# Performance work log

Measured on AMD Instinct MI355X. Metric: run time of the kernel, lower is better.

The kernel has to match this reference:

```python
import jax, jax.numpy as jnp
import numpy as np

N, IN_DIM, HID, HEADS = 4096, 256, 64, 8


def setup_inputs() -> dict:
    key = jax.random.key(0)
    ks = jax.random.split(key, 9)
    feats = jax.random.normal(ks[0], (N, IN_DIM), dtype=jnp.float32)
    adj = jax.random.bernoulli(ks[1], 0.01, (N, N)) | jnp.eye(N, dtype=bool)
    def lin(k, fin, fout):
        return jax.random.normal(k, (fin, fout), dtype=jnp.float32) / np.float32(np.sqrt(fin))
    return {
        "features": feats,
        "adjacency": adj,
        "W_in": lin(ks[2], IN_DIM, HID * HEADS),            # linear (no bias)
        "W_out": lin(ks[3], HID * HEADS, HID),              # out_proj
        "b_out": jnp.zeros((HID,), jnp.float32),
        "W_c1": lin(ks[4], HID * 2, HID),                   # classifier[1]
        "b_c1": jnp.zeros((HID,), jnp.float32),
        "W_c2": lin(ks[5], HID, 1),                         # classifier[3]
        "b_c2": jnp.zeros((1,), jnp.float32),
    }


def reference(features, adjacency, W_in, W_out, b_out, W_c1, b_c1, W_c2, b_c2):
    n = features.shape[0]
    # multi-head GAT: [H, N, D]
    proj = (features @ W_in).reshape(n, HEADS, HID).transpose(1, 0, 2)
    logits = jnp.einsum('hnd,hmd->hnm', proj, proj) / np.float32(np.sqrt(HID))
    logits = jnp.where(adjacency[None, :, :], logits, -jnp.inf)
    attn = jax.nn.softmax(logits, axis=-1)
    attended = jnp.einsum('hnm,hmd->hnd', attn, proj)
    attended = attended.transpose(1, 0, 2).reshape(n, HEADS * HID)
    node_states = attended @ W_out + b_out
    # memory_bank is None -> concat with zeros
    fused = jnp.concatenate([node_states, jnp.zeros_like(node_states)], axis=-1)
    h = jax.nn.gelu(fused, approximate=False) @ W_c1 + b_c1
    scores = (jax.nn.gelu(h, approximate=False) @ W_c2 + b_c2).squeeze(-1)
    # attention heatmap: masked row-normalized cosine similarity
    eps = np.float32(1e-8)
    norm = jnp.maximum(jnp.linalg.norm(node_states, axis=-1, keepdims=True), eps)
    xn = node_states / norm
    sim = jnp.where(adjacency, xn @ xn.T, 0.0)
    heatmap = sim / (sim.sum(axis=-1, keepdims=True) + eps)
    return scores, heatmap
```

## Files before the change

kernel.cpp:

```cpp
#include <hip/hip_runtime.h>
#include <math.h>

constexpr int NN    = 4096;
constexpr int INDIM = 256;
constexpr int HID   = 64;
constexpr int HEADS = 8;
constexpr int HH    = HID * HEADS;
constexpr int DMAX  = 256;
constexpr int PROJ_BLOCKS = 512;

typedef float        vfloat4 __attribute__((ext_vector_type(4)));
typedef unsigned int vuint4  __attribute__((ext_vector_type(4)));

__device__ __forceinline__ float gelu_exact(float x) {
    return 0.5f * x * (1.0f + erff(x * 0.70710678118654752f));
}

__device__ __forceinline__ float wave_reduce64(float v) {
    v += __shfl_xor(v, 32); v += __shfl_xor(v, 16); v += __shfl_xor(v, 8);
    v += __shfl_xor(v, 4);  v += __shfl_xor(v, 2);  v += __shfl_xor(v, 1);
    return v;
}

__global__ __launch_bounds__(256) void prep_kernel(
    const void* __restrict__ adjv,
    const float* __restrict__ A, const float* __restrict__ B,
    float* __restrict__ projT,
    unsigned short* __restrict__ nbr_g, int* __restrict__ deg_g) {
    __shared__ float Bs[128][64];
    __shared__ int wsum[4], u8w[4];
    const int pb = blockIdx.x, t = threadIdx.x;
    const int wv = t >> 6, lane = t & 63;

    if (pb < PROJ_BLOCKS) {
        const int bx = pb & 7, by = pb >> 3;
        const int tx = t & 15, ty = t >> 4;
        const float* ap0 = A + (size_t)(by * 64 + ty * 4 + 0) * INDIM;
        const float* ap1 = A + (size_t)(by * 64 + ty * 4 + 1) * INDIM;
        const float* ap2 = A + (size_t)(by * 64 + ty * 4 + 2) * INDIM;
        const float* ap3 = A + (size_t)(by * 64 + ty * 4 + 3) * INDIM;
        float acc[4][4] = {{0.0f}};

        for (int kh = 0; kh < 2; ++kh) {
            #pragma unroll
            for (int i = t; i < 128 * 16; i += 256) {
                const int k = i >> 4, c4 = (i & 15) * 4;
                *reinterpret_cast<float4*>(&Bs[k][c4]) =
                    *reinterpret_cast<const float4*>(
                        B + (size_t)(kh * 128 + k) * HH + bx * 64 + c4);
            }
            __syncthreads();
            #pragma unroll 2
            for (int k = 0; k < 128; k += 4) {
                const int ka = kh * 128 + k;
                float4 av[4];
                av[0] = *reinterpret_cast<const float4*>(ap0 + ka);
                av[1] = *reinterpret_cast<const float4*>(ap1 + ka);
                av[2] = *reinterpret_cast<const float4*>(ap2 + ka);
                av[3] = *reinterpret_cast<const float4*>(ap3 + ka);
                float4 bv[4];
                #pragma unroll
                for (int kk = 0; kk < 4; ++kk)
                    bv[kk] = *reinterpret_cast<const float4*>(&Bs[k + kk][tx * 4]);
                #pragma unroll
                for (int i = 0; i < 4; ++i) {
                    const float a0 = av[i].x, a1 = av[i].y, a2 = av[i].z, a3 = av[i].w;
                    acc[i][0] += a0 * bv[0].x + a1 * bv[1].x + a2 * bv[2].x + a3 * bv[3].x;
                    acc[i][1] += a0 * bv[0].y + a1 * bv[1].y + a2 * bv[2].y + a3 * bv[3].y;
                    acc[i][2] += a0 * bv[0].z + a1 * bv[1].z + a2 * bv[2].z + a3 * bv[3].z;
                    acc[i][3] += a0 * bv[0].w + a1 * bv[1].w + a2 * bv[2].w + a3 * bv[3].w;
                }
            }
            __syncthreads();
        }
        #pragma unroll
        for (int i = 0; i < 4; ++i) {
            float4 o = {acc[i][0], acc[i][1], acc[i][2], acc[i][3]};
            *reinterpret_cast<float4*>(
                projT + ((size_t)bx * NN + by * 64 + ty * 4 + i) * HID + tx * 4) = o;
        }
    } else {
        const int n = pb - PROJ_BLOCKS;
        const vuint4 pw = __builtin_nontemporal_load(
            reinterpret_cast<const vuint4*>(adjv) + t);
        int u8loc = 0;
        #pragma unroll
        for (int a = 0; a < 4; ++a) {
            const unsigned w = pw[a];
            if (((w & ~0x01010101u) == 0u) && ((w & 0xFFFFFF00u) != 0u)) u8loc = 1;
        }
        const unsigned long long wb = __ballot(u8loc);
        if (lane == 0) u8w[wv] = (wb != 0ull);
        __syncthreads();
        const bool isU8 = (u8w[0] | u8w[1] | u8w[2] | u8w[3]) != 0;

        unsigned int nzmask = 0;
        if (isU8) {
            const vuint4 r = __builtin_nontemporal_load(
                reinterpret_cast<const vuint4*>(
                    (const unsigned char*)adjv + (size_t)n * NN + 16 * t));
            #pragma unroll
            for (int a = 0; a < 4; ++a)
                #pragma unroll
                for (int j = 0; j < 4; ++j)
                    if ((r[a] >> (8 * j)) & 0xFFu) nzmask |= 1u << (a * 4 + j);
        } else {
            const vuint4* p = reinterpret_cast<const vuint4*>(
                (const unsigned int*)adjv + (size_t)n * NN + 16 * t);
            #pragma unroll
            for (int a = 0; a < 4; ++a) {
                const vuint4 r = __builtin_nontemporal_load(p + a);
                if (r[0]) nzmask |= 1u << (a * 4 + 0);
                if (r[1]) nzmask |= 1u << (a * 4 + 1);
                if (r[2]) nzmask |= 1u << (a * 4 + 2);
                if (r[3]) nzmask |= 1u << (a * 4 + 3);
            }
        }
        const int c = __popc(nzmask);
        int x = c;
        #pragma unroll
        for (int d = 1; d < 64; d <<= 1) {
            int y = __shfl_up(x, d);
            if (lane >= d) x += y;
        }
        if (lane == 63) wsum[wv] = x;
        __syncthreads();
        int base = 0;
        #pragma unroll
        for (int i = 0; i < 4; ++i)
            if (i < wv) base += wsum[i];
        const int deg = min(wsum[0] + wsum[1] + wsum[2] + wsum[3], DMAX);
        if (t == 0) deg_g[n] = deg;
        int o = base + x - c;
        unsigned int mm = nzmask;
        while (mm) {
            const int j = __ffs(mm) - 1;
            mm &= mm - 1;
            if (o < DMAX) nbr_g[(size_t)n * DMAX + o] = (unsigned short)(16 * t + j);
            ++o;
        }
    }
}

__global__ __launch_bounds__(256) void attn_kernel(
    const float* __restrict__ projT,
    const unsigned short* __restrict__ nbr_g, const int* __restrict__ deg_g,
    float* __restrict__ attended) {
    __shared__ unsigned short nl[4][DMAX];
    const int b = blockIdx.x, t = threadIdx.x;
    const int wv = t >> 6, lane = t & 63;
    const int h = b & 7;
    const int n = (b >> 3) * 4 + wv;
    const int deg = deg_g[n];

    *reinterpret_cast<ushort4*>(&nl[wv][lane * 4]) =
        *reinterpret_cast<const ushort4*>(nbr_g + (size_t)n * DMAX + lane * 4);

    const float* tab = projT + (size_t)h * NN * HID;
    const int g = lane >> 3, dl = (lane & 7) * 8;

    float q[8];
    {
        const float4 a = *reinterpret_cast<const float4*>(tab + (size_t)n * HID + dl);
        const float4 bq = *reinterpret_cast<const float4*>(tab + (size_t)n * HID + dl + 4);
        q[0] = a.x;  q[1] = a.y;  q[2] = a.z;  q[3] = a.w;
        q[4] = bq.x; q[5] = bq.y; q[6] = bq.z; q[7] = bq.w;
    }

    float l = 0.0f;
    float acc[8] = {0.f, 0.f, 0.f, 0.f, 0.f, 0.f, 0.f, 0.f};
    #pragma unroll 2
    for (int c0 = 0; c0 < deg; c0 += 8) {
        const int c = c0 + g;
        const int idx = nl[wv][min(c, deg - 1)];
        const float* kp = tab + (size_t)idx * HID + dl;
        const float4 ka = *reinterpret_cast<const float4*>(kp);
        const float4 kb = *reinterpret_cast<const float4*>(kp + 4);
        float kf[8] = {ka.x, ka.y, ka.z, ka.w, kb.x, kb.y, kb.z, kb.w};
        float s = q[0]*kf[0] + q[1]*kf[1] + q[2]*kf[2] + q[3]*kf[3] +
                  q[4]*kf[4] + q[5]*kf[5] + q[6]*kf[6] + q[7]*kf[7];
        s += __shfl_xor(s, 1); s += __shfl_xor(s, 2); s += __shfl_xor(s, 4);
        const float w = (c < deg) ? expf(s * 0.125f) : 0.0f;
        l += w;
        #pragma unroll
        for (int i = 0; i < 8; ++i) acc[i] += w * kf[i];
    }
    l += __shfl_xor(l, 8); l += __shfl_xor(l, 16); l += __shfl_xor(l, 32);
    #pragma unroll
    for (int i = 0; i < 8; ++i) {
        acc[i] += __shfl_xor(acc[i], 8);
        acc[i] += __shfl_xor(acc[i], 16);
        acc[i] += __shfl_xor(acc[i], 32);
    }
    const float invL = 1.0f / l;
    if (g == 0) {
        float4 o1 = {acc[0] * invL, acc[1] * invL, acc[2] * invL, acc[3] * invL};
        float4 o2 = {acc[4] * invL, acc[5] * invL, acc[6] * invL, acc[7] * invL};
        float* dst = attended + (size_t)n * HH + h * HID + dl;
        *reinterpret_cast<float4*>(dst)     = o1;
        *reinterpret_cast<float4*>(dst + 4) = o2;
    }
}

__global__ __launch_bounds__(256) void post_kernel(
    const float* __restrict__ attended,
    const float* __restrict__ W_out, const float* __restrict__ b_out,
    const float* __restrict__ W_c1, const float* __restrict__ b_c1,
    const float* __restrict__ W_c2, const float* __restrict__ b_c2,
    float* __restrict__ scores, float* __restrict__ xn) {
    __shared__ float qv2[4][HH];
    __shared__ float red[4][16][HID];
    __shared__ float nsbuf[4][HID];
    const int n0 = blockIdx.x * 4, t = threadIdx.x;
    const int wv = t >> 6, lane = t & 63;

    #pragma unroll
    for (int nd = 0; nd < 4; ++nd) {
        qv2[nd][t]       = attended[(size_t)(n0 + nd) * HH + t];
        qv2[nd][t + 256] = attended[(size_t)(n0 + nd) * HH + t + 256];
    }
    __syncthreads();

    {
        const int part = t >> 4, jq = (t & 15) * 4;
        float4 p0 = {0,0,0,0}, p1 = {0,0,0,0}, p2 = {0,0,0,0}, p3 = {0,0,0,0};
        const int d0 = part * 32;
        #pragma unroll 4
        for (int d = d0; d < d0 + 32; ++d) {
            const float4 w4 = *reinterpret_cast<const float4*>(&W_out[d * HID + jq]);
            const float q0 = qv2[0][d], q1 = qv2[1][d];
            const float q2 = qv2[2][d], q3 = qv2[3][d];
            p0.x += q0 * w4.x; p0.y += q0 * w4.y; p0.z += q0 * w4.z; p0.w += q0 * w4.w;
            p1.x += q1 * w4.x; p1.y += q1 * w4.y; p1.z += q1 * w4.z; p1.w += q1 * w4.w;
            p2.x += q2 * w4.x; p2.y += q2 * w4.y; p2.z += q2 * w4.z; p2.w += q2 * w4.w;
            p3.x += q3 * w4.x; p3.y += q3 * w4.y; p3.z += q3 * w4.z; p3.w += q3 * w4.w;
        }
        *reinterpret_cast<float4*>(&red[0][part][jq]) = p0;
        *reinterpret_cast<float4*>(&red[1][part][jq]) = p1;
        *reinterpret_cast<float4*>(&red[2][part][jq]) = p2;
        *reinterpret_cast<float4*>(&red[3][part][jq]) = p3;
    }
    __syncthreads();
    {
        float s = b_out[lane];
        #pragma unroll
        for (int pp = 0; pp < 16; ++pp) s += red[wv][pp][lane];
        nsbuf[wv][lane] = s;
    }
    __syncthreads();

    const int n = n0 + wv;
    const float ns = nsbuf[wv][lane];
    const float s2 = wave_reduce64(ns * ns);
    const float invn = 1.0f / fmaxf(sqrtf(s2), 1e-8f);
    xn[(size_t)n * HID + lane] = ns * invn;
    const float gb = gelu_exact(ns);
    __syncthreads();
    nsbuf[wv][lane] = gb;
    float hv = b_c1[lane];
    for (int i = 0; i < HID; ++i) hv += nsbuf[wv][i] * W_c1[i * HID + lane];
    const float hb = gelu_exact(hv);
    const float sc_ = wave_reduce64(hb * W_c2[lane]);
    if (lane == 0) scores[n] = sc_ + b_c2[0];
}

__global__ __launch_bounds__(256) void heat_kernel(
    const unsigned short* __restrict__ nbr_g, const int* __restrict__ deg_g,
    const float* __restrict__ xn, float* __restrict__ heat) {
    __shared__ float srow[NN];
    __shared__ float simv[DMAX];
    __shared__ unsigned short nl[DMAX];
    __shared__ float inv_s;
    const int n = blockIdx.x, t = threadIdx.x;
    const int wv = t >> 6, lane = t & 63;
    const int deg = deg_g[n];

    float4* sr4 = (float4*)srow;
    const float4 z4 = {0.f, 0.f, 0.f, 0.f};
    for (int i = t; i < NN / 4; i += 256) sr4[i] = z4;
    if (t < deg) nl[t] = nbr_g[(size_t)n * DMAX + t];

    const int g = lane >> 3, dl = (lane & 7) * 8;
    float xq[8];
    {
        const float4 a = *reinterpret_cast<const float4*>(xn + (size_t)n * HID + dl);
        const float4 b = *reinterpret_cast<const float4*>(xn + (size_t)n * HID + dl + 4);
        xq[0] = a.x; xq[1] = a.y; xq[2] = a.z; xq[3] = a.w;
        xq[4] = b.x; xq[5] = b.y; xq[6] = b.z; xq[7] = b.w;
    }
    __syncthreads();

    for (int c0 = wv * 8; c0 < deg; c0 += 32) {
        const int c = c0 + g;
        const int m = nl[min(c, deg - 1)];
        const float* xp = xn + (size_t)m * HID + dl;
        const float4 xa = *reinterpret_cast<const float4*>(xp);
        const float4 xb = *reinterpret_cast<const float4*>(xp + 4);
        float s = xq[0]*xa.x + xq[1]*xa.y + xq[2]*xa.z + xq[3]*xa.w +
                  xq[4]*xb.x + xq[5]*xb.y + xq[6]*xb.z + xq[7]*xb.w;
        s += __shfl_xor(s, 1); s += __shfl_xor(s, 2); s += __shfl_xor(s, 4);
        if (c < deg && (lane & 7) == 0) { srow[m] = s; simv[c] = s; }
    }
    __syncthreads();
    if (t < 64) {
        float ps = 0.0f;
        for (int c = t; c < deg; c += 64) ps += simv[c];
        ps = wave_reduce64(ps);
        if (t == 0) inv_s = 1.0f / (ps + 1e-8f);
    }
    __syncthreads();
    const float inv = inv_s;
    vfloat4* hr4 = (vfloat4*)(heat + (size_t)n * NN);
    for (int i = t; i < NN / 4; i += 256) {
        float4 v = sr4[i];
        vfloat4 nv = {v.x * inv, v.y * inv, v.z * inv, v.w * inv};
        __builtin_nontemporal_store(nv, hr4 + i);
    }
}

extern "C" void kernel_launch(void* const* d_in, const int* in_sizes, int n_in,
                              void* d_out, int out_size, void* d_ws, size_t ws_size,
                              hipStream_t stream) {
    const float* features = (const float*)d_in[0];
    const void*  adj      = d_in[1];
    const float* W_in     = (const float*)d_in[2];
    const float* W_out    = (const float*)d_in[3];
    const float* b_out    = (const float*)d_in[4];
    const float* W_c1     = (const float*)d_in[5];
    const float* b_c1     = (const float*)d_in[6];
    const float* W_c2     = (const float*)d_in[7];
    const float* b_c2     = (const float*)d_in[8];

    float* scores = (float*)d_out;
    float* heat   = (float*)d_out + NN;

    float*          projT    = (float*)d_ws;
    float*          attended = projT + (size_t)HEADS * NN * HID;
    float*          xn       = attended + (size_t)NN * HH;
    unsigned short* nbr_g    = (unsigned short*)(xn + (size_t)NN * HID);
    int*            deg_g    = (int*)(nbr_g + (size_t)NN * DMAX);

    prep_kernel<<<PROJ_BLOCKS + NN, 256, 0, stream>>>(adj, features, W_in,
                                                      projT, nbr_g, deg_g);
    attn_kernel<<<NN * HEADS / 4, 256, 0, stream>>>(projT, nbr_g, deg_g, attended);
    post_kernel<<<NN / 4, 256, 0, stream>>>(attended, W_out, b_out, W_c1, b_c1,
                                            W_c2, b_c2, scores, xn);
    heat_kernel<<<NN, 256, 0, stream>>>(nbr_g, deg_g, xn, heat);
}
```

Measured before the change: 201.6 us.

## Zero heatmap in prep kernel and scatter only neighbor entries in heat kernel

The dense zero-fill of the 64 MB heatmap moves into the adjacency-scan blocks of the prep kernel, where it can overlap with the adjacency reads. The heat kernel now assigns one wave per row and scatters only the normalized similarity values at neighbor positions, dropping the shared-memory row buffer and the block-wide syncs. This cuts the heat kernel's full-row LDS staging and streaming writes, but it adds scattered single-float nontemporal stores and more write traffic in the prep phase.

```diff
diff --git a/kernel.cpp b/kernel.cpp
--- a/kernel.cpp
+++ b/kernel.cpp
@@ -26,7 +26,8 @@
     const void* __restrict__ adjv,
     const float* __restrict__ A, const float* __restrict__ B,
     float* __restrict__ projT,
-    unsigned short* __restrict__ nbr_g, int* __restrict__ deg_g) {
+    unsigned short* __restrict__ nbr_g, int* __restrict__ deg_g,
+    float* __restrict__ heat) {
     __shared__ float Bs[128][64];
     __shared__ int wsum[4], u8w[4];
     const int pb = blockIdx.x, t = threadIdx.x;
@@ -81,6 +82,13 @@
         }
     } else {
         const int n = pb - PROJ_BLOCKS;
+        {
+            const vfloat4 z = {0.f, 0.f, 0.f, 0.f};
+            vfloat4* hr = (vfloat4*)(heat + (size_t)n * NN);
+            #pragma unroll
+            for (int i = 0; i < 4; ++i)
+                __builtin_nontemporal_store(z, hr + t + 256 * i);
+        }
         const vuint4 pw = __builtin_nontemporal_load(
             reinterpret_cast<const vuint4*>(adjv) + t);
         int u8loc = 0;
@@ -267,18 +275,15 @@
 __global__ __launch_bounds__(256) void heat_kernel(
     const unsigned short* __restrict__ nbr_g, const int* __restrict__ deg_g,
     const float* __restrict__ xn, float* __restrict__ heat) {
-    __shared__ float srow[NN];
-    __shared__ float simv[DMAX];
-    __shared__ unsigned short nl[DMAX];
-    __shared__ float inv_s;
-    const int n = blockIdx.x, t = threadIdx.x;
+    __shared__ float simv[4][DMAX];
+    __shared__ unsigned short nl[4][DMAX];
+    const int t = threadIdx.x;
     const int wv = t >> 6, lane = t & 63;
+    const int n = blockIdx.x * 4 + wv;
     const int deg = deg_g[n];
 
-    float4* sr4 = (float4*)srow;
-    const float4 z4 = {0.f, 0.f, 0.f, 0.f};
-    for (int i = t; i < NN / 4; i += 256) sr4[i] = z4;
-    if (t < deg) nl[t] = nbr_g[(size_t)n * DMAX + t];
+    *reinterpret_cast<ushort4*>(&nl[wv][lane * 4]) =
+        *reinterpret_cast<const ushort4*>(nbr_g + (size_t)n * DMAX + lane * 4);
 
     const int g = lane >> 3, dl = (lane & 7) * 8;
     float xq[8];
@@ -288,33 +293,27 @@
         xq[0] = a.x; xq[1] = a.y; xq[2] = a.z; xq[3] = a.w;
         xq[4] = b.x; xq[5] = b.y; xq[6] = b.z; xq[7] = b.w;
     }
-    __syncthreads();
-
-    for (int c0 = wv * 8; c0 < deg; c0 += 32) {
+
+    for (int c0 = 0; c0 < deg; c0 += 8) {
         const int c = c0 + g;
-        const int m = nl[min(c, deg - 1)];
+        const int m = nl[wv][min(c, deg - 1)];
         const float* xp = xn + (size_t)m * HID + dl;
         const float4 xa = *reinterpret_cast<const float4*>(xp);
         const float4 xb = *reinterpret_cast<const float4*>(xp + 4);
         float s = xq[0]*xa.x + xq[1]*xa.y + xq[2]*xa.z + xq[3]*xa.w +
                   xq[4]*xb.x + xq[5]*xb.y + xq[6]*xb.z + xq[7]*xb.w;
         s += __shfl_xor(s, 1); s += __shfl_xor(s, 2); s += __shfl_xor(s, 4);
-        if (c < deg && (lane & 7) == 0) { srow[m] = s; simv[c] = s; }
-    }
-    __syncthreads();
-    if (t < 64) {
-        float ps = 0.0f;
-        for (int c = t; c < deg; c += 64) ps += simv[c];
-        ps = wave_reduce64(ps);
-        if (t == 0) inv_s = 1.0f / (ps + 1e-8f);
-    }
-    __syncthreads();
-    const float inv = inv_s;
-    vfloat4* hr4 = (vfloat4*)(heat + (size_t)n * NN);
-    for (int i = t; i < NN / 4; i += 256) {
-        float4 v = sr4[i];
-        vfloat4 nv = {v.x * inv, v.y * inv, v.z * inv, v.w * inv};
-        __builtin_nontemporal_store(nv, hr4 + i);
+        if (c < deg && (lane & 7) == 0) simv[wv][c] = s;
+    }
+
+    float ps = 0.0f;
+    for (int c = lane; c < deg; c += 64) ps += simv[wv][c];
+    ps = wave_reduce64(ps);
+    const float inv = 1.0f / (ps + 1e-8f);
+
+    for (int c = lane; c < deg; c += 64) {
+        __builtin_nontemporal_store(simv[wv][c] * inv,
+                                    heat + (size_t)n * NN + nl[wv][c]);
     }
 }
 
@@ -341,9 +340,9 @@
     int*            deg_g    = (int*)(nbr_g + (size_t)NN * DMAX);
 
     prep_kernel<<<PROJ_BLOCKS + NN, 256, 0, stream>>>(adj, features, W_in,
-                                                      projT, nbr_g, deg_g);
+                                                      projT, nbr_g, deg_g, heat);
     attn_kernel<<<NN * HEADS / 4, 256, 0, stream>>>(projT, nbr_g, deg_g, attended);
     post_kernel<<<NN / 4, 256, 0, stream>>>(attended, W_out, b_out, W_c1, b_c1,
                                             W_c2, b_c2, scores, xn);
-    heat_kernel<<<NN, 256, 0, stream>>>(nbr_g, deg_g, xn, heat);
-}
+    heat_kernel<<<NN / 4, 256, 0, stream>>>(nbr_g, deg_g, xn, heat);
+}
```

Result: slower. 208.4 us (+3.4%).

## Store projection row-major and process all heads per node in one block

Applied to the files above, without the earlier changes.

The projection is now written in natural node-major [N, HEADS*HID] layout instead of head-major [HEADS, N, HID]. The attention kernel launches one block per node, with each of the 256 threads owning two channels across all 8 heads. Each neighbor's full 2KB row is then read with coalesced float2 loads, and the neighbor list is staged once for all heads. The trade-off is a sequential loop over neighbors with one neighbor per iteration and 5-step shuffle reductions per neighbor, where the old code processed 8 neighbors in parallel per wave.

```diff
diff --git a/kernel.cpp b/kernel.cpp
--- a/kernel.cpp
+++ b/kernel.cpp
@@ -25,7 +25,7 @@
 __global__ __launch_bounds__(256) void prep_kernel(
     const void* __restrict__ adjv,
     const float* __restrict__ A, const float* __restrict__ B,
-    float* __restrict__ projT,
+    float* __restrict__ P,
     unsigned short* __restrict__ nbr_g, int* __restrict__ deg_g) {
     __shared__ float Bs[128][64];
     __shared__ int wsum[4], u8w[4];
@@ -77,7 +77,7 @@
         for (int i = 0; i < 4; ++i) {
             float4 o = {acc[i][0], acc[i][1], acc[i][2], acc[i][3]};
             *reinterpret_cast<float4*>(
-                projT + ((size_t)bx * NN + by * 64 + ty * 4 + i) * HID + tx * 4) = o;
+                P + (size_t)(by * 64 + ty * 4 + i) * HH + bx * 64 + tx * 4) = o;
         }
     } else {
         const int n = pb - PROJ_BLOCKS;
@@ -143,63 +143,34 @@
 }
 
 __global__ __launch_bounds__(256) void attn_kernel(
-    const float* __restrict__ projT,
+    const float* __restrict__ P,
     const unsigned short* __restrict__ nbr_g, const int* __restrict__ deg_g,
     float* __restrict__ attended) {
-    __shared__ unsigned short nl[4][DMAX];
-    const int b = blockIdx.x, t = threadIdx.x;
-    const int wv = t >> 6, lane = t & 63;
-    const int h = b & 7;
-    const int n = (b >> 3) * 4 + wv;
+    __shared__ unsigned short nl[DMAX];
+    const int n = blockIdx.x, t = threadIdx.x;
     const int deg = deg_g[n];
 
-    *reinterpret_cast<ushort4*>(&nl[wv][lane * 4]) =
-        *reinterpret_cast<const ushort4*>(nbr_g + (size_t)n * DMAX + lane * 4);
-
-    const float* tab = projT + (size_t)h * NN * HID;
-    const int g = lane >> 3, dl = (lane & 7) * 8;
-
-    float q[8];
-    {
-        const float4 a = *reinterpret_cast<const float4*>(tab + (size_t)n * HID + dl);
-        const float4 bq = *reinterpret_cast<const float4*>(tab + (size_t)n * HID + dl + 4);
-        q[0] = a.x;  q[1] = a.y;  q[2] = a.z;  q[3] = a.w;
-        q[4] = bq.x; q[5] = bq.y; q[6] = bq.z; q[7] = bq.w;
-    }
-
-    float l = 0.0f;
-    float acc[8] = {0.f, 0.f, 0.f, 0.f, 0.f, 0.f, 0.f, 0.f};
-    #pragma unroll 2
-    for (int c0 = 0; c0 < deg; c0 += 8) {
-        const int c = c0 + g;
-        const int idx = nl[wv][min(c, deg - 1)];
-        const float* kp = tab + (size_t)idx * HID + dl;
-        const float4 ka = *reinterpret_cast<const float4*>(kp);
-        const float4 kb = *reinterpret_cast<const float4*>(kp + 4);
-        float kf[8] = {ka.x, ka.y, ka.z, ka.w, kb.x, kb.y, kb.z, kb.w};
-        float s = q[0]*kf[0] + q[1]*kf[1] + q[2]*kf[2] + q[3]*kf[3] +
-                  q[4]*kf[4] + q[5]*kf[5] + q[6]*kf[6] + q[7]*kf[7];
+    if (t < 64)
+        *reinterpret_cast<ushort4*>(&nl[t * 4]) =
+            *reinterpret_cast<const ushort4*>(nbr_g + (size_t)n * DMAX + t * 4);
+    const float2 q2 = *reinterpret_cast<const float2*>(P + (size_t)n * HH + 2 * t);
+    __syncthreads();
+
+    float l = 0.0f, ax = 0.0f, ay = 0.0f;
+    #pragma unroll 4
+    for (int c = 0; c < deg; ++c) {
+        const int m = nl[c];
+        const float2 k2 = *reinterpret_cast<const float2*>(P + (size_t)m * HH + 2 * t);
+        float s = q2.x * k2.x + q2.y * k2.y;
         s += __shfl_xor(s, 1); s += __shfl_xor(s, 2); s += __shfl_xor(s, 4);
-        const float w = (c < deg) ? expf(s * 0.125f) : 0.0f;
+        s += __shfl_xor(s, 8); s += __shfl_xor(s, 16);
+        const float w = expf(s * 0.125f);
         l += w;
-        #pragma unroll
-        for (int i = 0; i < 8; ++i) acc[i] += w * kf[i];
-    }
-    l += __shfl_xor(l, 8); l += __shfl_xor(l, 16); l += __shfl_xor(l, 32);
-    #pragma unroll
-    for (int i = 0; i < 8; ++i) {
-        acc[i] += __shfl_xor(acc[i], 8);
-        acc[i] += __shfl_xor(acc[i], 16);
-        acc[i] += __shfl_xor(acc[i], 32);
+        ax += w * k2.x; ay += w * k2.y;
     }
     const float invL = 1.0f / l;
-    if (g == 0) {
-        float4 o1 = {acc[0] * invL, acc[1] * invL, acc[2] * invL, acc[3] * invL};
-        float4 o2 = {acc[4] * invL, acc[5] * invL, acc[6] * invL, acc[7] * invL};
-        float* dst = attended + (size_t)n * HH + h * HID + dl;
-        *reinterpret_cast<float4*>(dst)     = o1;
-        *reinterpret_cast<float4*>(dst + 4) = o2;
-    }
+    const float2 o = {ax * invL, ay * invL};
+    *reinterpret_cast<float2*>(attended + (size_t)n * HH + 2 * t) = o;
 }
 
 __global__ __launch_bounds__(256) void post_kernel(
@@ -334,15 +305,15 @@
     float* scores = (float*)d_out;
     float* heat   = (float*)d_out + NN;
 
-    float*          projT    = (float*)d_ws;
-    float*          attended = projT + (size_t)HEADS * NN * HID;
+    float*          P        = (float*)d_ws;
+    float*          attended = P + (size_t)NN * HH;
     float*          xn       = attended + (size_t)NN * HH;
     unsigned short* nbr_g    = (unsigned short*)(xn + (size_t)NN * HID);
     int*            deg_g    = (int*)(nbr_g + (size_t)NN * DMAX);
 
     prep_kernel<<<PROJ_BLOCKS + NN, 256, 0, stream>>>(adj, features, W_in,
-                                                      projT, nbr_g, deg_g);
-    attn_kernel<<<NN * HEADS / 4, 256, 0, stream>>>(projT, nbr_g, deg_g, attended);
+                                                      P, nbr_g, deg_g);
+    attn_kernel<<<NN, 256, 0, stream>>>(P, nbr_g, deg_g, attended);
     post_kernel<<<NN / 4, 256, 0, stream>>>(attended, W_out, b_out, W_c1, b_c1,
                                             W_c2, b_c2, scores, xn);
     heat_kernel<<<NN, 256, 0, stream>>>(nbr_g, deg_g, xn, heat);
```

After: 239.2 us. +18.7%, slower.
